# Performance work log

Measured on AMD Instinct MI355X. Metric: run time of the kernel, lower is better.

Reference implementation:

```python
import jax, jax.numpy as jnp
import numpy as np

W = 64          # word_embedding_size
ES = 64         # entity_embedding_size
H = 4           # head_num
DH = W // H
K = 3           # convolution_num
NW, NQ, NE, NR = 50000, 20000, 200000, 100000
LQ, LR, EP, B = 8, 16, 500000, 1024
D = ES + W      # propagated entity feature dim


def _mhsa_mean(x, Wq, bq, Wk, bk, Wv, bv, Wo, bo):
    # x: [N, L, W] -> [N, W]; standard multi-head self-attention then mean over L
    N, L, _ = x.shape
    q = (x @ Wq + bq).reshape(N, L, H, DH)
    k = (x @ Wk + bk).reshape(N, L, H, DH)
    v = (x @ Wv + bv).reshape(N, L, H, DH)
    s = jnp.einsum('nlhd,nmhd->nhlm', q, k) / jnp.sqrt(jnp.asarray(DH, x.dtype))
    a = jax.nn.softmax(s, axis=-1)
    o = jnp.einsum('nhlm,nmhd->nlhd', a, v).reshape(N, L, W)
    return (o @ Wo + bo).mean(axis=1)


def setup_inputs() -> dict:
    key = jax.random.key(0)
    ks = jax.random.split(key, 20)
    f = jnp.float32
    inp = {
        'word_emb': jax.random.normal(ks[0], (NW, W), f) * 0.02,
        'entity_emb': jax.random.normal(ks[1], (NE, ES), f) * 0.02,
        'Wq': jax.random.normal(ks[2], (W, W), f) * (1.0 / np.sqrt(W)),
        'bq': jnp.zeros((W,), f),
        'Wk': jax.random.normal(ks[3], (W, W), f) * (1.0 / np.sqrt(W)),
        'bk': jnp.zeros((W,), f),
        'Wv': jax.random.normal(ks[4], (W, W), f) * (1.0 / np.sqrt(W)),
        'bv': jnp.zeros((W,), f),
        'Wo': jax.random.normal(ks[5], (W, W), f) * (1.0 / np.sqrt(W)),
        'bo': jnp.zeros((W,), f),
        'review_words': jax.random.randint(ks[6], (NR, LR), 0, NW),
        'query_words_graph': jax.random.randint(ks[7], (NQ, LQ), 0, NW),
        'profile_dst': jax.random.randint(ks[8], (NR,), 0, NE),
        'pur_src': jax.random.randint(ks[9], (EP,), 0, NE),
        'pur_dst': jax.random.randint(ks[10], (EP,), 0, NE),
        'pur_qid': jax.random.randint(ks[11], (EP,), 0, NQ),
        'users': jax.random.randint(ks[12], (B,), 0, NE),
        'items': jax.random.randint(ks[13], (B,), 0, NE),
        'negs': jax.random.randint(ks[14], (B,), 0, NE),
        'query_words': jax.random.randint(ks[15], (B, LQ), 0, NW),
    }
    return inp


def reference(word_emb, entity_emb, Wq, bq, Wk, bk, Wv, bv, Wo, bo,
              review_words, query_words_graph, profile_dst,
              pur_src, pur_dst, pur_qid, users, items, negs, query_words):
    seg = jax.ops.segment_sum
    attn = lambda x: _mhsa_mean(x, Wq, bq, Wk, bk, Wv, bv, Wo, bo)
    we = word_emb.at[0].set(0.0)  # padding_idx=0

    # composes: word -> review / query (mailbox attention reduce)
    rev_h = attn(we[review_words])              # [NR, W]
    q_h = attn(we[query_words_graph])           # [NQ, W]
    q_e0 = jnp.concatenate([jnp.zeros((NQ, ES), we.dtype), q_h], axis=-1)  # [NQ, D]

    # profiles: review -> entity, mean by in-degree
    deg_p = jnp.clip(seg(jnp.ones((NR,), we.dtype), profile_dst, num_segments=NE), 1.0)[:, None]
    prof = seg(rev_h, profile_dst, num_segments=NE) / deg_p   # [NE, W]
    e = jnp.concatenate([entity_emb, prof], axis=-1)          # e_0: [NE, D]

    # deg_i = out_deg(purchased) + out_deg(purchased_by), clamped
    ones_e = jnp.ones((EP,), we.dtype)
    deg_i = jnp.clip(seg(ones_e, pur_src, num_segments=NE)
                     + seg(ones_e, pur_dst, num_segments=NE), 1.0)[:, None]
    inv = 1.0 / jnp.sqrt(deg_i)                               # [NE, 1]

    es = [e]
    for _ in range(K):
        msg = e * inv                                         # e_k / sqrt(deg_i)
        m_pur = e[pur_src] + q_e0[pur_qid] * inv[pur_src]     # msg_u_i UDF
        nxt = seg(m_pur, pur_dst, num_segments=NE) \
            + seg(msg[pur_dst], pur_src, num_segments=NE)     # purchased_by (reverse)
        e = nxt * inv
        es.append(e)
    efin = sum(es) / (K + 1)                                  # [NE, D]

    # batch scoring
    u = efin[users]
    qb = attn(we[query_words])                                # [B, W]
    p = u + jnp.concatenate([jnp.zeros((B, ES), we.dtype), qb], axis=-1)
    pos = jnp.sum(p * efin[items], axis=-1)
    neg = jnp.sum(p * efin[negs], axis=-1)
    loss = -jnp.mean(jax.nn.log_sigmoid(pos - neg))           # BPR loss
    return loss
```

## Files before the change

kernel.cpp:

```cpp
#include <hip/hip_runtime.h>
#include <hip/hip_fp8.h>
#include <cstdint>

#define CDIV(a,b) (((a)+(b)-1)/(b))

typedef __attribute__((ext_vector_type(8))) short bf16x8;
typedef __attribute__((ext_vector_type(4))) float f32x4;
typedef __attribute__((ext_vector_type(8))) float f32x8;
typedef __attribute__((ext_vector_type(4))) _Float16 half4;
typedef __attribute__((ext_vector_type(8))) _Float16 half8;

#define QK_SCALE 32.0f
#define SCORE_SCALE (0.25f / (QK_SCALE * QK_SCALE))
#define EXP2_C (SCORE_SCALE * 1.44269504089f)

#define ES_SCALE 64.0f

__device__ __forceinline__ float bf2f(short s) {
    return __builtin_bit_cast(float, ((unsigned)(unsigned short)s) << 16);
}
__device__ __forceinline__ short rtne(float f) {
    const unsigned u = __builtin_bit_cast(unsigned, f);
    return (short)((u + 0x7fffu + ((u >> 16) & 1u)) >> 16);
}
__device__ __forceinline__ unsigned pack2r(float lo, float hi) {
    return (unsigned)(unsigned short)rtne(lo) | ((unsigned)(unsigned short)rtne(hi) << 16);
}
__device__ __forceinline__ float fp8tof(unsigned char b) {
    __hip_fp8_e4m3 t; t.__x = b; return (float)t;
}
__device__ __forceinline__ unsigned char ftofp8(float f) {
    __hip_fp8_e4m3 t(f); return t.__x;
}
__device__ __forceinline__ f32x8 fp8x8tof32(long v) {
    union { long l; unsigned char b[8]; } u; u.l = v;
    f32x8 r;
    #pragma unroll
    for (int j = 0; j < 8; ++j) r[j] = fp8tof(u.b[j]);
    return r;
}
__device__ __forceinline__ long f32x8tofp8(f32x8 a) {
    union { long l; unsigned char b[8]; } u;
    #pragma unroll
    for (int j = 0; j < 8; ++j) u.b[j] = ftofp8(a[j]);
    return u.l;
}

template<int CTRL>
__device__ __forceinline__ float dpp_add(float x) {
    const int t = __builtin_amdgcn_update_dpp(0, __builtin_bit_cast(int, x),
                                              CTRL, 0xf, 0xf, true);
    return x + __builtin_bit_cast(float, t);
}
__device__ __forceinline__ float rowsum16(float x) {
    x = dpp_add<0x108>(x);
    x = dpp_add<0x104>(x);
    x = dpp_add<0x102>(x);
    x = dpp_add<0x101>(x);
    return x;
}


__device__ __forceinline__ void prep_body(int bid,
    const float* __restrict__ we, const short* __restrict__ Wt,
    const float* __restrict__ bq, const float* __restrict__ bk,
    const float* __restrict__ bv, unsigned char* __restrict__ WQKV, int NW)
{
    const int wave = threadIdx.x >> 6;
    const int lane = threadIdx.x & 63;
    const int quad = lane >> 4;
    const int lm   = lane & 15;
    const int ntiles = CDIV(NW, 16);

    bf16x8 bfr[3][4][2];
    #pragma unroll
    for (int p = 0; p < 3; ++p)
        #pragma unroll
        for (int nt = 0; nt < 4; ++nt)
            #pragma unroll
            for (int kh = 0; kh < 2; ++kh)
                bfr[p][nt][kh] = *(const bf16x8*)(Wt + ((p*64 + nt*16 + lm)*64) + kh*32 + quad*8);
    float bias[3][4];
    #pragma unroll
    for (int nt = 0; nt < 4; ++nt) {
        bias[0][nt] = bq[nt*16 + lm];
        bias[1][nt] = bk[nt*16 + lm];
        bias[2][nt] = bv[nt*16 + lm];
    }

    #pragma unroll
    for (int t = 0; t < 4; ++t) {
        const int tile = (bid*4 + wave)*4 + t;
        if (tile >= ntiles) return;
        const int wb = tile*16;
        int w = wb + lm;
        if (w >= NW) w = NW - 1;
        const float* xr = we + (size_t)w*64;
        union { unsigned u[4]; bf16x8 v; } a0, a1;
        const float4 f0 = *(const float4*)(xr + quad*8);
        const float4 f1 = *(const float4*)(xr + quad*8 + 4);
        const float4 f2 = *(const float4*)(xr + 32 + quad*8);
        const float4 f3 = *(const float4*)(xr + 32 + quad*8 + 4);
        a0.u[0] = pack2r(f0.x, f0.y); a0.u[1] = pack2r(f0.z, f0.w);
        a0.u[2] = pack2r(f1.x, f1.y); a0.u[3] = pack2r(f1.z, f1.w);
        a1.u[0] = pack2r(f2.x, f2.y); a1.u[1] = pack2r(f2.z, f2.w);
        a1.u[2] = pack2r(f3.x, f3.y); a1.u[3] = pack2r(f3.z, f3.w);
        if (w == 0) {
            a0.u[0]=0u; a0.u[1]=0u; a0.u[2]=0u; a0.u[3]=0u;
            a1.u[0]=0u; a1.u[1]=0u; a1.u[2]=0u; a1.u[3]=0u;
        }
        #pragma unroll
        for (int p = 0; p < 3; ++p) {
            #pragma unroll
            for (int nt = 0; nt < 4; ++nt) {
                f32x4 c = {bias[p][nt], bias[p][nt], bias[p][nt], bias[p][nt]};
                c = __builtin_amdgcn_mfma_f32_16x16x32_bf16(a0.v, bfr[p][nt][0], c, 0, 0, 0);
                c = __builtin_amdgcn_mfma_f32_16x16x32_bf16(a1.v, bfr[p][nt][1], c, 0, 0, 0);
                #pragma unroll
                for (int r = 0; r < 4; ++r) {
                    const int w2 = wb + quad*4 + r;
                    if (w2 < NW) {
                        unsigned char* rowo = WQKV + (size_t)w2*192;
                        const int base = (p == 2) ? 128 : (p == 0) ? 64 : 0;
                        rowo[base + nt*16 + lm] = ftofp8(c[r] * QK_SCALE);
                    }
                }
            }
        }
    }
}

__device__ __forceinline__ void fill_body(int bid,
    const int* __restrict__ src, const int* __restrict__ dst,
    const int* __restrict__ qid,
    const int* __restrict__ offC,
    const int* __restrict__ rankD, const int* __restrict__ rankS,
    int2* __restrict__ cmb2, int EP)
{
    const int t = bid*256 + threadIdx.x;
    if (t >= EP) return;
    const int s = src[t], d = dst[t];
    const int p1 = offC[d] + rankD[t];
    int2 e1; e1.x = s; e1.y = qid[t];
    cmb2[p1] = e1;
    const int p2 = offC[s] + rankS[t];
    int2 e2; e2.x = d | (int)0x80000000; e2.y = 0;
    cmb2[p2] = e2;
}

__device__ __forceinline__ void expand_body(int bid, int nb, unsigned targ,
    const int* __restrict__ slist, const int* __restrict__ pn,
    const int* __restrict__ offC, const int* __restrict__ endC,
    const int2* __restrict__ cmb2, unsigned* __restrict__ lev,
    int* __restrict__ dl1, int* __restrict__ dn1,
    int* __restrict__ dl2, int* __restrict__ dn2)
{
    const int n = *pn;
    const int stride = nb * 256;
    for (int t = bid*256 + threadIdx.x; t < n; t += stride) {
        const int v = slist[t];
        const int b0 = offC[v], e0 = endC[v];
        for (int i = b0; i < e0; ++i) {
            const int u = cmb2[i].x & 0x7fffffff;
            const unsigned old = atomicMax(&lev[u], targ);
            if (old < targ) {
                dl1[atomicAdd(dn1, 1)] = u;
                if (dl2) dl2[atomicAdd(dn2, 1)] = u;
            }
        }
    }
}

__device__ __forceinline__ void finalize_body(int bid,
    const float* __restrict__ emb, const float* __restrict__ prof,
    unsigned char* __restrict__ e8, float* __restrict__ inv,
    const unsigned* __restrict__ deg_p, const unsigned* __restrict__ cntC, int NE)
{
    const int t = bid*256 + threadIdx.x;
    const int v = t >> 5;
    if (v >= NE) return;
    const int c = (t & 31) * 4;
    float4 ev;
    if (c < 64) {
        ev = *(const float4*)&emb[(size_t)v*64 + c];
    } else {
        ev = *(const float4*)&prof[(size_t)v*64 + (c - 64)];
        const unsigned dp = deg_p[v];
        const float r = 1.0f / (float)(dp > 1u ? dp : 1u);
        ev.x *= r; ev.y *= r; ev.z *= r; ev.w *= r;
    }
    union { unsigned u; unsigned char b[4]; } pk;
    pk.b[0] = ftofp8(ev.x * ES_SCALE);
    pk.b[1] = ftofp8(ev.y * ES_SCALE);
    pk.b[2] = ftofp8(ev.z * ES_SCALE);
    pk.b[3] = ftofp8(ev.w * ES_SCALE);
    *(unsigned*)&e8[(size_t)v*128 + c] = pk.u;
    if (c == 0) {
        const unsigned di = cntC[v];
        inv[v] = 1.0f / sqrtf((float)(di > 1u ? di : 1u));
    }
}

__device__ __forceinline__ void gather_body(int bid,
    const unsigned char* __restrict__ e8, const int* __restrict__ users,
    const int* __restrict__ items, const int* __restrict__ negs,
    float* __restrict__ acc, int B)
{
    const int t = bid*256 + threadIdx.x;
    const int r = t >> 4;
    if (r >= 3*B) return;
    const int c = (t & 15) * 8;
    const int which = r / B, b = r - which*B;
    const int idx = (which == 0) ? users[b] : (which == 1) ? items[b] : negs[b];
    const long ev = *(const long*)&e8[(size_t)idx*128 + c];
    f32x8 a = *(const f32x8*)&acc[(size_t)r*128 + c];
    a += fp8x8tof32(ev);
    *(f32x8*)&acc[(size_t)r*128 + c] = a;
}

__device__ __forceinline__ void prop1_body(int bid, int nb,
    const unsigned char* __restrict__ e_cur, const _Float16* __restrict__ q_h16,
    const float* __restrict__ inv,
    const int* __restrict__ offC, const int* __restrict__ endC,
    const int2* __restrict__ cmb2,
    const int* __restrict__ list, const int* __restrict__ pn,
    unsigned char* __restrict__ e_nxt, _Float16* __restrict__ qc)
{
    const int n = *pn;
    const int stride = nb * 256;
    for (int t = bid*256 + threadIdx.x; (t >> 4) < n; t += stride) {
        const int v = list[t >> 4];
        const int c = (t & 15) * 8;
        const bool qlane = (c >= 64);
        f32x8 a  = {0.f,0.f,0.f,0.f,0.f,0.f,0.f,0.f};
        f32x8 qa = {0.f,0.f,0.f,0.f,0.f,0.f,0.f,0.f};
        const int b0 = offC[v], e0 = endC[v];
        for (int i = b0; i < e0; ++i) {
            const int2 e = cmb2[i];
            const int u = e.x & 0x7fffffff;
            const float w = (e.x < 0) ? inv[u] : 1.0f;
            a += fp8x8tof32(*(const long*)&e_cur[(size_t)u*128 + c]) * w;
            if (e.x >= 0 && qlane) {
                const half8 qh = *(const half8*)&q_h16[(size_t)e.y*64 + (c - 64)];
                qa += __builtin_convertvector(qh, f32x8) * inv[u];
            }
        }
        if (qlane) {
            qa *= ES_SCALE;
            *(half8*)&qc[(size_t)v*64 + (c - 64)] = __builtin_convertvector(qa, half8);
            a += qa;
        }
        a *= inv[v];
        *(long*)&e_nxt[(size_t)v*128 + c] = f32x8tofp8(a);
    }
}

__device__ __forceinline__ void prop_list_body(int bid, int nb,
    const unsigned char* __restrict__ e_cur, const _Float16* __restrict__ qc,
    const float* __restrict__ inv,
    const int* __restrict__ offC, const int* __restrict__ endC,
    const int2* __restrict__ cmb2,
    const int* __restrict__ list, const int* __restrict__ pn,
    unsigned char* __restrict__ e_nxt)
{
    const int n = *pn;
    const int stride = nb * 256;
    for (int t = bid*256 + threadIdx.x; (t >> 4) < n; t += stride) {
        const int v = list[t >> 4];
        const int c = (t & 15) * 8;
        f32x8 a = {0.f,0.f,0.f,0.f,0.f,0.f,0.f,0.f};
        if (c >= 64) {
            const half8 q = *(const half8*)&qc[(size_t)v*64 + (c - 64)];
            a = __builtin_convertvector(q, f32x8);
        }
        const int b0 = offC[v], e0 = endC[v];
        int un = (b0 < e0) ? cmb2[b0].x : 0;
        for (int i = b0; i < e0; ++i) {
            const int uc = un;
            if (i + 1 < e0) un = cmb2[i + 1].x;
            const int u = uc & 0x7fffffff;
            const long es = *(const long*)&e_cur[(size_t)u*128 + c];
            const float w = (uc < 0) ? inv[u] : 1.0f;
            a += fp8x8tof32(es) * w;
        }
        a *= inv[v];
        *(long*)&e_nxt[(size_t)v*128 + c] = f32x8tofp8(a);
    }
}

struct TileRegs { int4 v0; long qf[4], kf[4]; };

__device__ __forceinline__ void load_tile(
    const unsigned char* __restrict__ WQKV, int w, int quad, TileRegs& t)
{
    const unsigned char* row = WQKV + (size_t)w * 192;
    t.v0 = *(const int4*)(row + 128 + quad*16);
    #pragma unroll
    for (int h = 0; h < 4; ++h) {
        if (quad < 2) {
            t.kf[h] = *(const long*)(row +      h*16 + quad*8);
            t.qf[h] = *(const long*)(row + 64 + h*16 + quad*8);
        } else {
            t.kf[h] = 0; t.qf[h] = 0;
        }
    }
}

template<int L, int MODE>
__device__ __forceinline__ void attn_body(
    unsigned char* __restrict__ smem,
    const unsigned char* __restrict__ WQKV, const int* __restrict__ words,
    const short* __restrict__ WoT, const float* __restrict__ bo,
    int N, void* __restrict__ outp, const int* __restrict__ sidx, int bid)
{
    constexpr int SPT = 16 / L;
    constexpr int SB  = 16 * SPT;
    unsigned char (*v_s)[16*80] = (unsigned char (*)[16*80])smem;
    float (*pbar_s)[64]         = (float (*)[64])(smem + 5120);
    float (*mo_s)[68]           = (float (*)[68])(smem + 6144);

    const int wave = threadIdx.x >> 6;
    const int lane = threadIdx.x & 63;
    const int quad = lane >> 4;
    const int lm   = lane & 15;
    const int tok_total = N * L;
    const float invL = 1.0f / ((float)L * QK_SCALE);

    int wid[4];
    #pragma unroll
    for (int t = 0; t < 4; ++t) {
        int tg = (bid*16 + wave*4 + t)*16 + lm;
        if (tg >= tok_total) tg = tok_total - 1;
        wid[t] = words[tg];
    }

    TileRegs cur, nxt;
    load_tile(WQKV, wid[0], quad, cur);

    #pragma unroll
    for (int ti = 0; ti < 4; ++ti) {
        if (ti < 3) load_tile(WQKV, wid[ti+1], quad, nxt);

        *(int4*)&v_s[wave][lm*80 + quad*16] = cur.v0;

        const bool mvalid = (SPT == 1) ? true : ((quad >> 1) == ((lm >> 3) & 1));

        #pragma unroll
        for (int h = 0; h < 4; ++h) {
            const f32x4 s4 = __builtin_amdgcn_mfma_f32_16x16x32_fp8_fp8(
                cur.kf[h], cur.qf[h], (f32x4){0.f,0.f,0.f,0.f}, 0, 0, 0);
            float sv0 = s4[0], sv1 = s4[1], sv2 = s4[2], sv3 = s4[3];
            if (!mvalid) { sv0 = sv1 = sv2 = sv3 = -3.0e38f; }
            float p0 = __builtin_amdgcn_exp2f(sv0*EXP2_C),
                  p1 = __builtin_amdgcn_exp2f(sv1*EXP2_C),
                  p2 = __builtin_amdgcn_exp2f(sv2*EXP2_C),
                  p3 = __builtin_amdgcn_exp2f(sv3*EXP2_C);
            float sm = p0+p1+p2+p3;
            sm += __shfl_xor(sm, 16, 64);
            sm += __shfl_xor(sm, 32, 64);
            const float rinv = __builtin_amdgcn_rcpf(sm);
            p0 *= rinv; p1 *= rinv; p2 *= rinv; p3 *= rinv;
            p0 = rowsum16(p0); p1 = rowsum16(p1);
            p2 = rowsum16(p2); p3 = rowsum16(p3);
            if (lm == 0) {
                pbar_s[wave][h*16 + quad*4 + 0] = p0 * invL;
                pbar_s[wave][h*16 + quad*4 + 1] = p1 * invL;
                pbar_s[wave][h*16 + quad*4 + 2] = p2 * invL;
                pbar_s[wave][h*16 + quad*4 + 3] = p3 * invL;
            }
        }

        #pragma unroll
        for (int s = 0; s < SPT; ++s) {
            f32x4 pb[4];
            #pragma unroll
            for (int j = 0; j < 4; ++j)
                pb[j] = *(const f32x4*)&pbar_s[wave][quad*16 + j*4];
            float o = 0.f;
            #pragma unroll
            for (int j2 = 0; j2 < L; ++j2) {
                const int m = s*L + j2;
                o += pb[m >> 2][m & 3] * fp8tof(v_s[wave][m*80 + lane]);
            }
            mo_s[(wave*4+ti)*SPT + s][lane] = o;
        }

        if (ti < 3) {
            cur.v0 = nxt.v0;
            #pragma unroll
            for (int h = 0; h < 4; ++h) { cur.qf[h] = nxt.qf[h]; cur.kf[h] = nxt.kf[h]; }
        }
    }
    __syncthreads();

    const int col = wave*16 + lm;
    const short* bT = WoT + col*64;
    const bf16x8 b0 = *(const bf16x8*)(bT + quad*8);
    const bf16x8 b1 = *(const bf16x8*)(bT + 32 + quad*8);
    const float boc = bo[col];
    #pragma unroll
    for (int rt = 0; rt < SPT; ++rt) {
        const float* ar = mo_s[rt*16 + lm];
        const float4 fA0 = *(const float4*)(ar + quad*8);
        const float4 fA1 = *(const float4*)(ar + quad*8 + 4);
        const float4 fA2 = *(const float4*)(ar + 32 + quad*8);
        const float4 fA3 = *(const float4*)(ar + 32 + quad*8 + 4);
        union { unsigned u[4]; bf16x8 v; } a0, a1;
        a0.u[0] = pack2r(fA0.x, fA0.y); a0.u[1] = pack2r(fA0.z, fA0.w);
        a0.u[2] = pack2r(fA1.x, fA1.y); a0.u[3] = pack2r(fA1.z, fA1.w);
        a1.u[0] = pack2r(fA2.x, fA2.y); a1.u[1] = pack2r(fA2.z, fA2.w);
        a1.u[2] = pack2r(fA3.x, fA3.y); a1.u[3] = pack2r(fA3.z, fA3.w);
        f32x4 c = {boc, boc, boc, boc};
        c = __builtin_amdgcn_mfma_f32_16x16x32_bf16(a0.v, b0, c, 0, 0, 0);
        c = __builtin_amdgcn_mfma_f32_16x16x32_bf16(a1.v, b1, c, 0, 0, 0);
        #pragma unroll
        for (int r = 0; r < 4; ++r) {
            const int seq = bid*SB + rt*16 + quad*4 + r;
            if (seq < N) {
                if (MODE == 0)
                    ((float*)outp)[(size_t)seq*64 + col] = c[r];
                else if (MODE == 1)
                    atomicAdd(&((float*)outp)[(size_t)sidx[seq]*64 + col], c[r]);
                else
                    ((_Float16*)outp)[(size_t)seq*64 + col] = (_Float16)c[r];
            }
        }
    }
}


__global__ __launch_bounds__(256) void misc_kernel(
    const int* __restrict__ src, const int* __restrict__ dst,
    unsigned* __restrict__ cntC, int* __restrict__ rankD, int* __restrict__ rankS,
    int EP,
    const int* __restrict__ pdst, unsigned* __restrict__ deg_p, int NR,
    const float* __restrict__ Wo, short* __restrict__ WoT,
    const float* __restrict__ Wq, const float* __restrict__ Wk,
    const float* __restrict__ Wv, short* __restrict__ Wt,
    const int* __restrict__ users, const int* __restrict__ items,
    const int* __restrict__ negs, int B, unsigned* __restrict__ lev,
    int* __restrict__ listS, int* __restrict__ list2, int* __restrict__ list1,
    int* __restrict__ nS, int* __restrict__ n2, int* __restrict__ n1,
    float4* __restrict__ prof_z, float4* __restrict__ acc_z,
    int prof4, int acc4, int nbM0)
{
    if ((int)blockIdx.x >= nbM0) {
        const int z = ((int)blockIdx.x - nbM0)*256 + (int)threadIdx.x;
        const float4 zero4 = {0.f, 0.f, 0.f, 0.f};
        if (z < prof4) prof_z[z] = zero4;
        else if (z - prof4 < acc4) acc_z[z - prof4] = zero4;
        return;
    }
    const int t = blockIdx.x*256 + threadIdx.x;
    if (t < EP) {
        const int s = src[t], d = dst[t];
        rankD[t] = (int)atomicAdd(&cntC[d], 1u);
        rankS[t] = (int)atomicAdd(&cntC[s], 1u);
    }
    if (t < NR) atomicAdd(&deg_p[pdst[t]], 1u);
    if (t < 4096) {
        const int j = t >> 6, k = t & 63;
        WoT[j*64 + k] = rtne(Wo[k*64 + j]);
    }
    if (t < 3*4096) {
        const int p = t >> 12, n = (t >> 6) & 63, k = t & 63;
        const float* W = (p==0) ? Wq : (p==1) ? Wk : Wv;
        Wt[t] = rtne(W[k*64 + n]);
    }
    if (t < 3*B) {
        const int which = t / B, b = t - which*B;
        const int v = (which == 0) ? users[b] : (which == 1) ? items[b] : negs[b];
        const unsigned old = atomicMax(&lev[v], 3u);
        if (old < 3u) {
            listS[atomicAdd(nS, 1)] = v;
            list2[atomicAdd(n2, 1)] = v;
            list1[atomicAdd(n1, 1)] = v;
        }
    }
}

#define SCAN_CHUNK 2048

__device__ __forceinline__ void scan_reduce_body(int b,
    const unsigned* __restrict__ cnt, unsigned* __restrict__ part, int n)
{
    const int base = b * SCAN_CHUNK;
    unsigned s = 0;
    #pragma unroll
    for (int i = 0; i < 8; ++i) {
        const int idx = base + i*256 + threadIdx.x;
        if (idx < n) s += cnt[idx];
    }
    #pragma unroll
    for (int off = 1; off < 64; off <<= 1) s += __shfl_xor(s, off, 64);
    __shared__ unsigned wsum[4];
    if ((threadIdx.x & 63) == 0) wsum[threadIdx.x >> 6] = s;
    __syncthreads();
    if (threadIdx.x == 0) part[b] = wsum[0]+wsum[1]+wsum[2]+wsum[3];
}

__global__ __launch_bounds__(256) void mega_scan_prep(
    const unsigned* __restrict__ cnt, unsigned* __restrict__ part, int n, int NB,
    const float* __restrict__ we, const short* __restrict__ Wt,
    const float* __restrict__ bq, const float* __restrict__ bk,
    const float* __restrict__ bv, unsigned char* __restrict__ WQKV, int NW)
{
    const int b = blockIdx.x;
    if (b < NB) scan_reduce_body(b, cnt, part, n);
    else        prep_body(b - NB, we, Wt, bq, bk, bv, WQKV, NW);
}

__global__ __launch_bounds__(256) void scan_final_kernel(
    const unsigned* __restrict__ cnt, const unsigned* __restrict__ part,
    int* __restrict__ off, int* __restrict__ cur, int n)
{
    const int b = blockIdx.x;
    __shared__ unsigned v[SCAN_CHUNK];
    __shared__ unsigned tsum[256];
    __shared__ unsigned wsum2[4];
    const int base = b * SCAN_CHUNK;
    const int t = threadIdx.x;
    unsigned pv = (t < b) ? part[t] : 0u;
    #pragma unroll
    for (int o = 1; o < 64; o <<= 1) pv += __shfl_xor(pv, o, 64);
    if ((t & 63) == 0) wsum2[t >> 6] = pv;
    #pragma unroll
    for (int i = 0; i < 8; ++i) {
        const int idx = base + i*256 + t;
        v[i*256 + t] = (idx < n) ? cnt[idx] : 0u;
    }
    __syncthreads();
    const unsigned pbase = wsum2[0]+wsum2[1]+wsum2[2]+wsum2[3];
    unsigned s = 0;
    #pragma unroll
    for (int i = 0; i < 8; ++i) s += v[t*8 + i];
    tsum[t] = s;
    __syncthreads();
    for (int d = 1; d < 256; d <<= 1) {
        const unsigned x = (t >= d) ? tsum[t-d] : 0u;
        __syncthreads();
        tsum[t] += x;
        __syncthreads();
    }
    unsigned run = ((t > 0) ? tsum[t-1] : 0u) + pbase;
    #pragma unroll
    for (int i = 0; i < 8; ++i) {
        const int idx = base + t*8 + i;
        if (idx < n) {
            const unsigned c = v[t*8+i];
            off[idx] = (int)run;
            cur[idx] = (int)(run + c);
            run += c;
        }
    }
}

__global__ __launch_bounds__(256) void mega_attn(
    const unsigned char* __restrict__ WQKV,
    const int* __restrict__ src, const int* __restrict__ dst,
    const int* __restrict__ qid, const int* __restrict__ offC,
    const int* __restrict__ rankD, const int* __restrict__ rankS,
    int2* __restrict__ cmb2, int EP, int nbF,
    const int* __restrict__ w1, int N1, float* __restrict__ o1,
    const int* __restrict__ sidx1, int nb1,
    const int* __restrict__ w2, int N2, _Float16* __restrict__ o2, int nb2,
    const int* __restrict__ w3, int N3, float* __restrict__ o3,
    const short* __restrict__ WoT, const float* __restrict__ bo)
{
    __shared__ __align__(16) unsigned char smem[6144 + 32*68*4];
    const int b = blockIdx.x;
    const int total = (int)gridDim.x;
    int W = (3*total)/5;
    if (W < nbF) W = nbF;
    const int wstart = total - W;
    int ba = b;
    if (b >= wstart) {
        const int local = b - wstart;
        const int f0 = (int)(((long)local * nbF) / W);
        const int f1 = (int)(((long)(local + 1) * nbF) / W);
        if (f1 > f0) {
            fill_body(f0, src, dst, qid, offC, rankD, rankS, cmb2, EP);
            return;
        }
        ba = b - f0;
    }
    if (ba < nb1)
        attn_body<16,1>(smem, WQKV, w1, WoT, bo, N1, o1, sidx1, ba);
    else if (ba < nb1 + nb2)
        attn_body<8,2>(smem, WQKV, w2, WoT, bo, N2, o2, nullptr, ba - nb1);
    else
        attn_body<8,0>(smem, WQKV, w3, WoT, bo, N3, o3, nullptr, ba - nb1 - nb2);
}

__global__ __launch_bounds__(256) void expand_kernel(
    unsigned targ, const int* __restrict__ slist, const int* __restrict__ pn,
    const int* __restrict__ offC, const int* __restrict__ endC,
    const int2* __restrict__ cmb2, unsigned* __restrict__ lev,
    int* __restrict__ dl1, int* __restrict__ dn1,
    int* __restrict__ dl2, int* __restrict__ dn2)
{
    expand_body(blockIdx.x, gridDim.x, targ, slist, pn, offC, endC, cmb2, lev,
                dl1, dn1, dl2, dn2);
}

__global__ __launch_bounds__(256) void mega_final(
    const int* __restrict__ list2, const int* __restrict__ n2,
    const int* __restrict__ offC, const int* __restrict__ endC,
    const int2* __restrict__ cmb2, unsigned* __restrict__ lev,
    int* __restrict__ list1, int* __restrict__ n1,
    const float* __restrict__ emb, const float* __restrict__ prof,
    unsigned char* __restrict__ e8, float* __restrict__ inv,
    const unsigned* __restrict__ deg_p, const unsigned* __restrict__ cntC, int NE)
{
    const int b = blockIdx.x;
    if (b < 256)
        expand_body(b, 256, 1u, list2, n2, offC, endC, cmb2, lev,
                    list1, n1, nullptr, nullptr);
    else
        finalize_body(b - 256, emb, prof, e8, inv, deg_p, cntC, NE);
}

__global__ __launch_bounds__(256) void mega_prop1(
    const unsigned char* __restrict__ e_cur, const _Float16* __restrict__ q_h16,
    const float* __restrict__ inv,
    const int* __restrict__ offC, const int* __restrict__ endC,
    const int2* __restrict__ cmb2,
    const int* __restrict__ list1, const int* __restrict__ n1,
    unsigned char* __restrict__ e_nxt, _Float16* __restrict__ qc,
    const int* __restrict__ users, const int* __restrict__ items,
    const int* __restrict__ negs, float* __restrict__ acc, int B)
{
    const int b = blockIdx.x;
    if (b < 2048) prop1_body(b, 2048, e_cur, q_h16, inv, offC, endC, cmb2,
                             list1, n1, e_nxt, qc);
    else          gather_body(b - 2048, e_cur, users, items, negs, acc, B);
}

__global__ __launch_bounds__(256) void mega_pg(
    const unsigned char* __restrict__ e_cur, const _Float16* __restrict__ qc,
    const float* __restrict__ inv,
    const int* __restrict__ offC, const int* __restrict__ endC,
    const int2* __restrict__ cmb2,
    const int* __restrict__ list2, const int* __restrict__ n2,
    unsigned char* __restrict__ e_nxt,
    const int* __restrict__ users, const int* __restrict__ items,
    const int* __restrict__ negs, float* __restrict__ acc, int B)
{
    const int b = blockIdx.x;
    if (b < 512) prop_list_body(b, 512, e_cur, qc, inv, offC, endC, cmb2,
                                list2, n2, e_nxt);
    else         gather_body(b - 512, e_cur, users, items, negs, acc, B);
}

__global__ __launch_bounds__(256) void prop_batch_kernel(
    const unsigned char* __restrict__ e_cur, const _Float16* __restrict__ qc,
    const float* __restrict__ inv,
    const int* __restrict__ offC, const int* __restrict__ endC,
    const int2* __restrict__ cmb2,
    const int* __restrict__ users, const int* __restrict__ items,
    const int* __restrict__ negs, float* __restrict__ acc, int B)
{
    const int t = blockIdx.x*256 + threadIdx.x;
    const int r = t >> 4;
    if (r >= 3*B) return;
    const int c = (t & 15) * 8;
    const int which = r / B, b = r - which*B;
    const int v = (which == 0) ? users[b] : (which == 1) ? items[b] : negs[b];
    f32x8 a = {0.f,0.f,0.f,0.f,0.f,0.f,0.f,0.f};
    if (c >= 64) {
        const half8 q = *(const half8*)&qc[(size_t)v*64 + (c - 64)];
        a = __builtin_convertvector(q, f32x8);
    }
    const int b0 = offC[v], e0 = endC[v];
    int un = (b0 < e0) ? cmb2[b0].x : 0;
    for (int i = b0; i < e0; ++i) {
        const int uc = un;
        if (i + 1 < e0) un = cmb2[i + 1].x;
        const int u = uc & 0x7fffffff;
        const long es = *(const long*)&e_cur[(size_t)u*128 + c];
        const float w = (uc < 0) ? inv[u] : 1.0f;
        a += fp8x8tof32(es) * w;
    }
    a *= inv[v];
    a += fp8x8tof32(*(const long*)&e_cur[(size_t)v*128 + c]);
    f32x8 ac = *(const f32x8*)&acc[(size_t)r*128 + c];
    ac += a;
    *(f32x8*)&acc[(size_t)r*128 + c] = ac;
}

__global__ __launch_bounds__(128) void loss_kernel(
    const float* __restrict__ acc, const float* __restrict__ qb,
    float* __restrict__ out, int B, float invB)
{
    const int b = blockIdx.x, d = threadIdx.x;
    const float u = acc[(size_t)b*128 + d] * (0.25f / ES_SCALE);
    const float p = u + (d >= 64 ? qb[(size_t)b*64 + (d - 64)] : 0.f);
    const float ei = acc[(size_t)(B + b)*128 + d];
    const float en = acc[(size_t)(2*B + b)*128 + d];
    float x = p * (ei - en) * (0.25f / ES_SCALE);
    #pragma unroll
    for (int off = 1; off < 64; off <<= 1) x += __shfl_xor(x, off, 64);
    __shared__ float wred[2];
    if ((threadIdx.x & 63) == 0) wred[threadIdx.x >> 6] = x;
    __syncthreads();
    if (threadIdx.x == 0) {
        const float xx = wred[0] + wred[1];
        const float ls = fminf(xx, 0.f) - log1pf(expf(-fabsf(xx)));
        atomicAdd(out, -ls * invB);
    }
}

extern "C" void kernel_launch(void* const* d_in, const int* in_sizes, int n_in,
                              void* d_out, int out_size, void* d_ws, size_t ws_size,
                              hipStream_t stream)
{
    const float* word_emb        = (const float*)d_in[0];
    const float* entity_emb      = (const float*)d_in[1];
    const float* Wq = (const float*)d_in[2];  const float* bq = (const float*)d_in[3];
    const float* Wk = (const float*)d_in[4];  const float* bk = (const float*)d_in[5];
    const float* Wv = (const float*)d_in[6];  const float* bv = (const float*)d_in[7];
    const float* Wo = (const float*)d_in[8];  const float* bo = (const float*)d_in[9];
    const int* review_words      = (const int*)d_in[10];
    const int* query_words_graph = (const int*)d_in[11];
    const int* profile_dst       = (const int*)d_in[12];
    const int* pur_src           = (const int*)d_in[13];
    const int* pur_dst           = (const int*)d_in[14];
    const int* pur_qid           = (const int*)d_in[15];
    const int* users             = (const int*)d_in[16];
    const int* items             = (const int*)d_in[17];
    const int* negs              = (const int*)d_in[18];
    const int* query_words       = (const int*)d_in[19];

    const int NW = in_sizes[0]  / 64;
    const int NE = in_sizes[1]  / 64;
    const int NR = in_sizes[10] / 16;
    const int NQ = in_sizes[11] / 8;
    const int EP = in_sizes[13];
    const int B  = in_sizes[16];
    const int NB = CDIV(NE, SCAN_CHUNK);

    char* ws = (char*)d_ws;
    size_t off = 0;
    auto alloc = [&](size_t bytes) -> char* {
        char* q = ws + off; off += (bytes + 255) & ~(size_t)255; return q;
    };
    float*         prof  = (float*)         alloc((size_t)NE*64*4);
    unsigned char* e8A   = (unsigned char*) alloc((size_t)NE*128);
    unsigned char* e8B   = (unsigned char*) alloc((size_t)NE*128);
    _Float16*      q_h16 = (_Float16*)      alloc((size_t)NQ*64*2);
    float*         qb    = (float*)         alloc((size_t)B*64*4);
    float*         acc   = (float*)         alloc((size_t)3*B*128*4);
    unsigned*  deg_p   = (unsigned*) alloc((size_t)NE*4);
    unsigned*  cntC    = (unsigned*) alloc((size_t)NE*4);
    unsigned*  lev     = (unsigned*) alloc((size_t)NE*4);
    int*       fcnt    = (int*)      alloc(256);
    int*       offC    = (int*)      alloc((size_t)NE*4);
    int*       curC    = (int*)      alloc((size_t)NE*4);
    int2*      cmb2    = (int2*)     alloc((size_t)2*EP*8);
    int*       rankD   = (int*)      alloc((size_t)EP*4);
    int*       rankS   = (int*)      alloc((size_t)EP*4);
    int*       listS   = (int*)      alloc((size_t)3*B*4);
    int*       list2   = (int*)      alloc((size_t)NE*4);
    int*       list1   = (int*)      alloc((size_t)NE*4);
    float*     inv     = (float*)    alloc((size_t)NE*4);
    unsigned*  part    = (unsigned*) alloc((size_t)NB*4);
    short*     WoT     = (short*)    alloc((size_t)64*64*2);
    short*     Wt      = (short*)    alloc((size_t)3*64*64*2);

    if (off > ws_size) return;

    unsigned char* WQKV = e8A;
    _Float16* qc = (_Float16*)prof;
    int* nS = fcnt; int* n2 = fcnt + 1; int* n1 = fcnt + 2;

    const size_t zlen = (size_t)((char*)fcnt - (char*)deg_p) + 256;
    hipMemsetAsync(deg_p, 0, zlen, stream);
    hipMemsetAsync(d_out, 0, (size_t)out_size*4, stream);

    const int nbM0  = CDIV(EP, 256);
    const int prof4 = NE*16;
    const int acc4  = 3*B*32;
    const int nbZ   = CDIV(prof4 + acc4, 256);
    misc_kernel<<<nbM0 + nbZ, 256, 0, stream>>>(pur_src, pur_dst, cntC,
        rankD, rankS, EP,
        profile_dst, deg_p, NR, Wo, WoT, Wq, Wk, Wv, Wt,
        users, items, negs, B, lev, listS, list2, list1, nS, n2, n1,
        (float4*)prof, (float4*)acc, prof4, acc4, nbM0);

    const int nbP = CDIV(CDIV(NW, 16), 16);
    mega_scan_prep<<<NB + nbP, 256, 0, stream>>>(cntC, part, NE, NB,
        word_emb, Wt, bq, bk, bv, WQKV, NW);
    scan_final_kernel<<<NB, 256, 0, stream>>>(cntC, part, offC, curC, NE);

    const int nbF = CDIV(EP, 256);
    const int nb1 = CDIV(NR, 16), nb2 = CDIV(NQ, 32), nb3 = CDIV(B, 32);
    mega_attn<<<nb1 + nb2 + nb3 + nbF, 256, 0, stream>>>(WQKV,
        pur_src, pur_dst, pur_qid, offC, rankD, rankS, cmb2, EP, nbF,
        review_words, NR, prof, profile_dst, nb1,
        query_words_graph, NQ, q_h16, nb2,
        query_words, B, qb, WoT, bo);

    expand_kernel<<<64, 256, 0, stream>>>(2u, listS, nS, offC, curC, cmb2, lev,
        list2, n2, list1, n1);

    mega_final<<<256 + CDIV(NE*32, 256), 256, 0, stream>>>(
        list2, n2, offC, curC, cmb2, lev, list1, n1,
        entity_emb, prof, e8A, inv, deg_p, cntC, NE);

    mega_prop1<<<2048 + CDIV(3*B*16, 256), 256, 0, stream>>>(
        e8A, q_h16, inv, offC, curC, cmb2, list1, n1, e8B, qc,
        users, items, negs, acc, B);

    mega_pg<<<512 + CDIV(3*B*16, 256), 256, 0, stream>>>(
        e8B, qc, inv, offC, curC, cmb2, list2, n2, e8A,
        users, items, negs, acc, B);

    prop_batch_kernel<<<CDIV(3*B*16, 256), 256, 0, stream>>>(e8A, qc, inv,
        offC, curC, cmb2, users, items, negs, acc, B);

    loss_kernel<<<B, 128, 0, stream>>>(acc, qb, (float*)d_out, B, 1.0f / (float)B);
}
```

Before: 436.9 us.

## Split entity finalize and move embedding half into earlier scan/prep launch

```diff
diff --git a/kernel.cpp b/kernel.cpp
--- a/kernel.cpp
+++ b/kernel.cpp
@@ -171,24 +171,15 @@
     }
 }
 
-__device__ __forceinline__ void finalize_body(int bid,
-    const float* __restrict__ emb, const float* __restrict__ prof,
-    unsigned char* __restrict__ e8, float* __restrict__ inv,
-    const unsigned* __restrict__ deg_p, const unsigned* __restrict__ cntC, int NE)
+__device__ __forceinline__ void femb_body(int bid,
+    const float* __restrict__ emb, unsigned char* __restrict__ e8,
+    float* __restrict__ inv, const unsigned* __restrict__ cntC, int NE)
 {
     const int t = bid*256 + threadIdx.x;
-    const int v = t >> 5;
+    const int v = t >> 4;
     if (v >= NE) return;
-    const int c = (t & 31) * 4;
-    float4 ev;
-    if (c < 64) {
-        ev = *(const float4*)&emb[(size_t)v*64 + c];
-    } else {
-        ev = *(const float4*)&prof[(size_t)v*64 + (c - 64)];
-        const unsigned dp = deg_p[v];
-        const float r = 1.0f / (float)(dp > 1u ? dp : 1u);
-        ev.x *= r; ev.y *= r; ev.z *= r; ev.w *= r;
-    }
+    const int c = (t & 15) * 4;
+    const float4 ev = *(const float4*)&emb[(size_t)v*64 + c];
     union { unsigned u; unsigned char b[4]; } pk;
     pk.b[0] = ftofp8(ev.x * ES_SCALE);
     pk.b[1] = ftofp8(ev.y * ES_SCALE);
@@ -199,6 +190,25 @@
         const unsigned di = cntC[v];
         inv[v] = 1.0f / sqrtf((float)(di > 1u ? di : 1u));
     }
+}
+
+__device__ __forceinline__ void fprof_body(int bid,
+    const float* __restrict__ prof, unsigned char* __restrict__ e8,
+    const unsigned* __restrict__ deg_p, int NE)
+{
+    const int t = bid*256 + threadIdx.x;
+    const int v = t >> 4;
+    if (v >= NE) return;
+    const int cc = (t & 15) * 4;
+    float4 ev = *(const float4*)&prof[(size_t)v*64 + cc];
+    const unsigned dp = deg_p[v];
+    const float r = ES_SCALE / (float)(dp > 1u ? dp : 1u);
+    union { unsigned u; unsigned char b[4]; } pk;
+    pk.b[0] = ftofp8(ev.x * r);
+    pk.b[1] = ftofp8(ev.y * r);
+    pk.b[2] = ftofp8(ev.z * r);
+    pk.b[3] = ftofp8(ev.w * r);
+    *(unsigned*)&e8[(size_t)v*128 + 64 + cc] = pk.u;
 }
 
 __device__ __forceinline__ void gather_body(int bid,
@@ -503,11 +513,14 @@
     const unsigned* __restrict__ cnt, unsigned* __restrict__ part, int n, int NB,
     const float* __restrict__ we, const short* __restrict__ Wt,
     const float* __restrict__ bq, const float* __restrict__ bk,
-    const float* __restrict__ bv, unsigned char* __restrict__ WQKV, int NW)
+    const float* __restrict__ bv, unsigned char* __restrict__ WQKV, int NW, int nbP,
+    const float* __restrict__ emb, unsigned char* __restrict__ e8,
+    float* __restrict__ inv, int NE)
 {
     const int b = blockIdx.x;
-    if (b < NB) scan_reduce_body(b, cnt, part, n);
-    else        prep_body(b - NB, we, Wt, bq, bk, bv, WQKV, NW);
+    if (b < NB)            scan_reduce_body(b, cnt, part, n);
+    else if (b < NB + nbP) prep_body(b - NB, we, Wt, bq, bk, bv, WQKV, NW);
+    else                   femb_body(b - NB - nbP, emb, e8, inv, cnt, NE);
 }
 
 __global__ __launch_bounds__(256) void scan_final_kernel(
@@ -608,16 +621,15 @@
     const int* __restrict__ offC, const int* __restrict__ endC,
     const int2* __restrict__ cmb2, unsigned* __restrict__ lev,
     int* __restrict__ list1, int* __restrict__ n1,
-    const float* __restrict__ emb, const float* __restrict__ prof,
-    unsigned char* __restrict__ e8, float* __restrict__ inv,
-    const unsigned* __restrict__ deg_p, const unsigned* __restrict__ cntC, int NE)
+    const float* __restrict__ prof, unsigned char* __restrict__ e8,
+    const unsigned* __restrict__ deg_p, int NE)
 {
     const int b = blockIdx.x;
     if (b < 256)
         expand_body(b, 256, 1u, list2, n2, offC, endC, cmb2, lev,
                     list1, n1, nullptr, nullptr);
     else
-        finalize_body(b - 256, emb, prof, e8, inv, deg_p, cntC, NE);
+        fprof_body(b - 256, prof, e8, deg_p, NE);
 }
 
 __global__ __launch_bounds__(256) void mega_prop1(
@@ -788,8 +800,10 @@
         (float4*)prof, (float4*)acc, prof4, acc4, nbM0);
 
     const int nbP = CDIV(CDIV(NW, 16), 16);
-    mega_scan_prep<<<NB + nbP, 256, 0, stream>>>(cntC, part, NE, NB,
-        word_emb, Wt, bq, bk, bv, WQKV, NW);
+    const int nbE = CDIV(NE*16, 256);
+    mega_scan_prep<<<NB + nbP + nbE, 256, 0, stream>>>(cntC, part, NE, NB,
+        word_emb, Wt, bq, bk, bv, WQKV, NW, nbP,
+        entity_emb, e8B, inv, NE);
     scan_final_kernel<<<NB, 256, 0, stream>>>(cntC, part, offC, curC, NE);
 
     const int nbF = CDIV(EP, 256);
@@ -803,19 +817,19 @@
     expand_kernel<<<64, 256, 0, stream>>>(2u, listS, nS, offC, curC, cmb2, lev,
         list2, n2, list1, n1);
 
-    mega_final<<<256 + CDIV(NE*32, 256), 256, 0, stream>>>(
+    mega_final<<<256 + nbE, 256, 0, stream>>>(
         list2, n2, offC, curC, cmb2, lev, list1, n1,
-        entity_emb, prof, e8A, inv, deg_p, cntC, NE);
+        prof, e8B, deg_p, NE);
 
     mega_prop1<<<2048 + CDIV(3*B*16, 256), 256, 0, stream>>>(
-        e8A, q_h16, inv, offC, curC, cmb2, list1, n1, e8B, qc,
+        e8B, q_h16, inv, offC, curC, cmb2, list1, n1, e8A, qc,
         users, items, negs, acc, B);
 
     mega_pg<<<512 + CDIV(3*B*16, 256), 256, 0, stream>>>(
-        e8B, qc, inv, offC, curC, cmb2, list2, n2, e8A,
+        e8A, qc, inv, offC, curC, cmb2, list2, n2, e8B,
         users, items, negs, acc, B);
 
-    prop_batch_kernel<<<CDIV(3*B*16, 256), 256, 0, stream>>>(e8A, qc, inv,
+    prop_batch_kernel<<<CDIV(3*B*16, 256), 256, 0, stream>>>(e8B, qc, inv,
         offC, curC, cmb2, users, items, negs, acc, B);
 
     loss_kernel<<<B, 128, 0, stream>>>(acc, qb, (float*)d_out, B, 1.0f / (float)B);
```

Result: slower. 468.2 us (+7.2%).
